# Kernel optimization log

Measured on AMD Instinct MI355X. Metric: run time of the kernel, lower is better.

Reference implementation:

```python
import jax, jax.numpy as jnp
import numpy as np


def dense_image_warp(image, flow):
    """Faithful port of tfa.image.dense_image_warp.

    output[b, y, x, c] = bilinear_sample(image[b], y - flow[b,y,x,0], x - flow[b,y,x,1])
    with floors clamped to [0, size-2] and alphas clamped to [0, 1]
    (matching tfa's _interpolate_bilinear clamping semantics).
    """
    B, H, W, C = image.shape
    gy = jnp.arange(H, dtype=image.dtype)[None, :, None]  # [1,H,1]
    gx = jnp.arange(W, dtype=image.dtype)[None, None, :]  # [1,1,W]
    qy = gy - flow[..., 0]  # [B,H,W]
    qx = gx - flow[..., 1]  # [B,H,W]

    fy = jnp.clip(jnp.floor(qy), 0.0, H - 2)
    fx = jnp.clip(jnp.floor(qx), 0.0, W - 2)
    ay = jnp.clip(qy - fy, 0.0, 1.0)[..., None]  # [B,H,W,1]
    ax = jnp.clip(qx - fx, 0.0, 1.0)[..., None]
    iy = fy.astype(jnp.int32)
    ix = fx.astype(jnp.int32)

    b_idx = jnp.arange(B)[:, None, None]  # [B,1,1]
    top_left = image[b_idx, iy, ix]          # [B,H,W,C]
    top_right = image[b_idx, iy, ix + 1]
    bottom_left = image[b_idx, iy + 1, ix]
    bottom_right = image[b_idx, iy + 1, ix + 1]

    interp_top = top_left + ax * (top_right - top_left)
    interp_bottom = bottom_left + ax * (bottom_right - bottom_left)
    return interp_top + ay * (interp_bottom - interp_top)


def setup_inputs() -> dict:
    key = jax.random.key(0)
    k1, k2 = jax.random.split(key)
    B, H, W, C = 8, 512, 512, 16
    image = jax.random.normal(k1, (B, H, W, C), dtype=jnp.float32)
    flow = jax.random.normal(k2, (B, H, W, 2), dtype=jnp.float32)
    return {"image": image, "flow": flow}


def reference(image, flow):
    return dense_image_warp(image, flow)
```

## Files before the change

kernel.cpp:

```cpp
#include <hip/hip_runtime.h>


__global__ __launch_bounds__(256) void warp_kernel(
    const float* __restrict__ img,
    const float* __restrict__ flow,
    float* __restrict__ out)
{
    const int tid = blockIdx.x * blockDim.x + threadIdx.x;

    const int cg = tid & 3;
    const int x  = (tid >> 2) & 511;
    const int y  = (tid >> 11) & 511;
    const int b  = tid >> 20;

    const int pix = (((b << 9) + y) << 9) + x;

    const float2 f = ((const float2*)flow)[pix];
    const float qy = (float)y - f.x;
    const float qx = (float)x - f.y;

    float fy = floorf(qy); fy = fminf(fmaxf(fy, 0.0f), 510.0f);
    float fx = floorf(qx); fx = fminf(fmaxf(fx, 0.0f), 510.0f);
    const float ay = fminf(fmaxf(qy - fy, 0.0f), 1.0f);
    const float ax = fminf(fmaxf(qx - fx, 0.0f), 1.0f);
    const int iy = (int)fy;
    const int ix = (int)fx;

    const float* p = img + ((size_t)((((b << 9) + iy) << 9) + ix)) * 16 + (cg << 2);

    const float4 tl = *(const float4*)(p);
    const float4 tr = *(const float4*)(p + 16);
    const float4 bl = *(const float4*)(p + 512 * 16);
    const float4 br = *(const float4*)(p + 512 * 16 + 16);

    float4 r;
    {
        float t, u;
        t = tl.x + ax * (tr.x - tl.x);
        u = bl.x + ax * (br.x - bl.x);
        r.x = t + ay * (u - t);
        t = tl.y + ax * (tr.y - tl.y);
        u = bl.y + ax * (br.y - bl.y);
        r.y = t + ay * (u - t);
        t = tl.z + ax * (tr.z - tl.z);
        u = bl.z + ax * (br.z - bl.z);
        r.z = t + ay * (u - t);
        t = tl.w + ax * (tr.w - tl.w);
        u = bl.w + ax * (br.w - bl.w);
        r.w = t + ay * (u - t);
    }

    ((float4*)out)[tid] = r;
}

extern "C" void kernel_launch(void* const* d_in, const int* in_sizes, int n_in,
                              void* d_out, int out_size, void* d_ws, size_t ws_size,
                              hipStream_t stream) {
    const float* img  = (const float*)d_in[0];
    const float* flow = (const float*)d_in[1];
    float* out = (float*)d_out;

    const int total = 8 * 512 * 512 * 4;
    const int block = 256;
    const int grid = total / block;
    warp_kernel<<<grid, block, 0, stream>>>(img, flow, out);
}
```

Before: 239.5 us.

## Tile warp kernel into 16x16 pixel blocks with XCD-aware block swizzle

Each 1024-thread block now covers a 16x16 pixel tile (4 channel groups per pixel) instead of a linear run of pixels along a row. Block IDs are remapped so that consecutive block IDs go to different batch images, which is meant to keep spatially adjacent tiles on the same XCD and its L2. The intended gain is better cache reuse of the bilinear neighbour gathers, since the 2D tile touches overlapping image rows. The cost is that output stores and flow loads are now only 64-byte-contiguous per row within a warp, where before they were fully linear.

```diff
diff --git a/kernel.cpp b/kernel.cpp
--- a/kernel.cpp
+++ b/kernel.cpp
@@ -1,17 +1,25 @@
 #include <hip/hip_runtime.h>
 
 
-__global__ __launch_bounds__(256) void warp_kernel(
+__global__ __launch_bounds__(1024) void warp_kernel(
     const float* __restrict__ img,
     const float* __restrict__ flow,
     float* __restrict__ out)
 {
-    const int tid = blockIdx.x * blockDim.x + threadIdx.x;
+    const int bid = blockIdx.x;
+    const int logical = ((bid & 7) << 10) + (bid >> 3);
 
-    const int cg = tid & 3;
-    const int x  = (tid >> 2) & 511;
-    const int y  = (tid >> 11) & 511;
-    const int b  = tid >> 20;
+    const int tx = logical & 31;
+    const int ty = (logical >> 5) & 31;
+    const int b  = logical >> 10;
+
+    const int t  = threadIdx.x;
+    const int cg = t & 3;
+    const int xx = (t >> 2) & 15;
+    const int yy = t >> 6;
+
+    const int x = (tx << 4) + xx;
+    const int y = (ty << 4) + yy;
 
     const int pix = (((b << 9) + y) << 9) + x;
 
@@ -35,22 +43,22 @@
 
     float4 r;
     {
-        float t, u;
-        t = tl.x + ax * (tr.x - tl.x);
-        u = bl.x + ax * (br.x - bl.x);
-        r.x = t + ay * (u - t);
-        t = tl.y + ax * (tr.y - tl.y);
-        u = bl.y + ax * (br.y - bl.y);
-        r.y = t + ay * (u - t);
-        t = tl.z + ax * (tr.z - tl.z);
-        u = bl.z + ax * (br.z - bl.z);
-        r.z = t + ay * (u - t);
-        t = tl.w + ax * (tr.w - tl.w);
-        u = bl.w + ax * (br.w - bl.w);
-        r.w = t + ay * (u - t);
+        float t0, u0;
+        t0 = tl.x + ax * (tr.x - tl.x);
+        u0 = bl.x + ax * (br.x - bl.x);
+        r.x = t0 + ay * (u0 - t0);
+        t0 = tl.y + ax * (tr.y - tl.y);
+        u0 = bl.y + ax * (br.y - bl.y);
+        r.y = t0 + ay * (u0 - t0);
+        t0 = tl.z + ax * (tr.z - tl.z);
+        u0 = bl.z + ax * (br.z - bl.z);
+        r.z = t0 + ay * (u0 - t0);
+        t0 = tl.w + ax * (tr.w - tl.w);
+        u0 = bl.w + ax * (br.w - bl.w);
+        r.w = t0 + ay * (u0 - t0);
     }
 
-    ((float4*)out)[tid] = r;
+    ((float4*)out)[(pix << 2) + cg] = r;
 }
 
 extern "C" void kernel_launch(void* const* d_in, const int* in_sizes, int n_in,
@@ -60,8 +68,7 @@
     const float* flow = (const float*)d_in[1];
     float* out = (float*)d_out;
 
-    const int total = 8 * 512 * 512 * 4;
-    const int block = 256;
-    const int grid = total / block;
+    const int block = 1024;
+    const int grid = (8 * 512 * 512 * 4) / block;
     warp_kernel<<<grid, block, 0, stream>>>(img, flow, out);
 }
```

New measurement: 243.1 us. No clear change (+1.5%).
